# Optimization experiments

Measured on AMD Instinct MI355X. Metric: run time of the kernel, lower is better.

The kernel has to match this reference:

```python
import jax, jax.numpy as jnp
import numpy as np

NUM_CLS = 81
N_ROI = 512
N_POS = 128
OUT = 7
SAMP = 2
SCALES = (0.25, 0.125, 0.0625, 0.03125)


def _roi_align(feat, rois, out, scale, samp=SAMP):
    # feat: [C,H,W]; rois: [N,4] (x1,y1,x2,y2) in image coords. torchvision-style
    # ROIAlign, aligned=False, avg pool over samp x samp bilinear samples per bin.
    C, H, W = feat.shape
    b = rois * scale
    x1, y1, x2, y2 = b[:, 0], b[:, 1], b[:, 2], b[:, 3]
    bw = jnp.maximum(x2 - x1, 1.0) / out
    bh = jnp.maximum(y2 - y1, 1.0) / out
    N = rois.shape[0]
    # sample offsets within a roi, in bin units: [out, samp]
    grid = jnp.arange(out, dtype=feat.dtype)[:, None] + (jnp.arange(samp, dtype=feat.dtype)[None, :] + 0.5) / samp
    px = x1[:, None, None] + grid[None] * bw[:, None, None]  # [N,out,samp]
    py = y1[:, None, None] + grid[None] * bh[:, None, None]
    # full sampling grid [N, out_y, out_x, samp_y, samp_x]
    PX = jnp.broadcast_to(px[:, None, :, None, :], (N, out, out, samp, samp))
    PY = jnp.broadcast_to(py[:, :, None, :, None], (N, out, out, samp, samp))
    valid = (PX > -1.0) & (PX < W) & (PY > -1.0) & (PY < H)
    x = jnp.clip(PX, 0.0, W - 1.0)
    y = jnp.clip(PY, 0.0, H - 1.0)
    x0f = jnp.floor(x)
    y0f = jnp.floor(y)
    lx = x - x0f
    ly = y - y0f
    x0 = x0f.astype(jnp.int32)
    y0 = y0f.astype(jnp.int32)
    x1i = jnp.minimum(x0 + 1, W - 1)
    y1i = jnp.minimum(y0 + 1, H - 1)
    def g(yi, xi):
        return feat[:, yi, xi]  # [C,N,out,out,samp,samp]
    v = (g(y0, x0) * (1 - ly) * (1 - lx) + g(y0, x1i) * (1 - ly) * lx
         + g(y1i, x0) * ly * (1 - lx) + g(y1i, x1i) * ly * lx)
    v = v * valid.astype(feat.dtype)
    pooled = v.mean(axis=(-1, -2))  # [C,N,out,out]
    return pooled.transpose(1, 0, 2, 3)  # [N,C,out,out]


def setup_inputs() -> dict:
    key = jax.random.key(0)
    ks = jax.random.split(key, 16)
    H_IMG, W_IMG = 800.0, 1024.0
    P2 = jax.random.normal(ks[0], (1, 256, 200, 256), jnp.float32)
    P3 = jax.random.normal(ks[1], (1, 256, 100, 128), jnp.float32)
    P4 = jax.random.normal(ks[2], (1, 256, 50, 64), jnp.float32)
    P5 = jax.random.normal(ks[3], (1, 256, 25, 32), jnp.float32)
    x1 = jax.random.uniform(ks[4], (N_ROI,)) * (W_IMG - 64.0)
    y1 = jax.random.uniform(ks[5], (N_ROI,)) * (H_IMG - 64.0)
    w = jax.random.uniform(ks[6], (N_ROI,), minval=16.0, maxval=512.0)
    h = jax.random.uniform(ks[7], (N_ROI,), minval=16.0, maxval=512.0)
    rois = jnp.stack([x1, y1, jnp.minimum(x1 + w, W_IMG - 1.0), jnp.minimum(y1 + h, H_IMG - 1.0)], axis=-1)
    label = jax.random.randint(ks[8], (N_ROI,), 0, NUM_CLS, dtype=jnp.int32)
    loc = jax.random.normal(ks[9], (N_POS, 4), jnp.float32) * 0.1
    s = 0.02
    return {
        'P2': P2, 'P3': P3, 'P4': P4, 'P5': P5,
        'rois': rois, 'label': label, 'loc': loc,
        'W1': jax.random.normal(ks[10], (256 * OUT * OUT, 1024), jnp.float32) * s,
        'b1': jnp.zeros((1024,), jnp.float32),
        'W2': jax.random.normal(ks[11], (1024, 1024), jnp.float32) * s,
        'b2': jnp.zeros((1024,), jnp.float32),
        'Wcls': jax.random.normal(ks[12], (1024, NUM_CLS), jnp.float32) * s,
        'bcls': jnp.zeros((NUM_CLS,), jnp.float32),
        'Wloc': jax.random.normal(ks[13], (1024, NUM_CLS * 4), jnp.float32) * s,
        'bloc': jnp.zeros((NUM_CLS * 4,), jnp.float32),
    }


def reference(P2, P3, P4, P5, rois, label, loc, W1, b1, W2, b2, Wcls, bcls, Wloc, bloc):
    feats = (P2[0], P3[0], P4[0], P5[0])
    # FPN level assignment: floor(4 + log2(sqrt(area)/224)).clamp(2,5) - 2
    area = (rois[:, 2] - rois[:, 0] + 1.0) * (rois[:, 3] - rois[:, 1] + 1.0)
    lvl = jnp.floor(4.0 + jnp.log(jnp.sqrt(area) / 224.0) / np.log(2.0))
    lvl = (jnp.clip(lvl, 2.0, 5.0) - 2.0).astype(jnp.int32)  # [N] in {0,1,2,3}
    onehot = jax.nn.one_hot(lvl, 4, dtype=rois.dtype)  # [N,4]
    # pool every roi at all 4 levels, select assigned level (same values as
    # the original per-level grouping + argsort re-ordering)
    pooled = jnp.stack([_roi_align(f, rois, OUT, s) for f, s in zip(feats, SCALES)])  # [4,N,C,7,7]
    x = jnp.einsum('lnchw,nl->nchw', pooled, onehot)
    # Fast head
    x = x.reshape(x.shape[0], -1)
    h = jax.nn.relu(x @ W1 + b1)
    h = jax.nn.relu(h @ W2 + b2)
    logits = h @ Wcls + bcls                    # [N, num_cls]
    locp = (h @ Wloc + bloc).reshape(-1, NUM_CLS, 4)
    # loss assembly
    logp = jax.nn.log_softmax(logits, axis=-1)
    cls_loss = -jnp.take_along_axis(logp, label[:, None], axis=1).mean()
    loc_train = locp[jnp.arange(N_POS), label[:N_POS]]  # class-indexed gather
    t = jnp.abs(loc_train - loc)
    sl1 = jnp.where(t < 1.0, 0.5 * t * t, t - 0.5)  # SmoothL1, sigma=1
    box_loss = sl1.sum() / float(N_ROI)
    return cls_loss + box_loss
```

## Files before the change

kernel.cpp:

```cpp
#include <hip/hip_runtime.h>
#include <hip/hip_bf16.h>
#include <math.h>

#define N_ROI 512
#define N_POS 128
#define NUM_CLS 81
#define KDIM 12544
#define HID 1024

typedef __bf16 bf16x8 __attribute__((ext_vector_type(8)));
typedef __bf16 bf16x4 __attribute__((ext_vector_type(4)));
typedef float f32x4 __attribute__((ext_vector_type(4)));

__device__ inline void gload16(const void* g, void* lds) {
  __builtin_amdgcn_global_load_lds(
      (const __attribute__((address_space(1))) void*)g,
      (__attribute__((address_space(3))) void*)lds, 16, 0, 0);
}

__global__ __launch_bounds__(256) void roi_align_kernel(
    const float* __restrict__ P2, const float* __restrict__ P3,
    const float* __restrict__ P4, const float* __restrict__ P5,
    const float* __restrict__ rois, __bf16* __restrict__ xout) {
  int n = blockIdx.x;
  int ch = blockIdx.y * 4 + (threadIdx.x >> 6);
  int lane = threadIdx.x & 63;

  float rx1 = rois[n * 4 + 0], ry1 = rois[n * 4 + 1];
  float rx2 = rois[n * 4 + 2], ry2 = rois[n * 4 + 3];
  float area = (rx2 - rx1 + 1.0f) * (ry2 - ry1 + 1.0f);
  float lf = floorf(4.0f + log2f(sqrtf(area) / 224.0f));
  lf = fminf(fmaxf(lf, 2.0f), 5.0f);
  int lvl = (int)lf - 2;

  const float scales[4] = {0.25f, 0.125f, 0.0625f, 0.03125f};
  const int   Hs[4] = {200, 100, 50, 25};
  const int   Ws[4] = {256, 128, 64, 32};
  const float* feats[4] = {P2, P3, P4, P5};
  float sc = scales[lvl];
  int H = Hs[lvl], W = Ws[lvl];
  const float* feat = feats[lvl];

  float bx1 = rx1 * sc, by1 = ry1 * sc;
  float bw = fmaxf(rx2 * sc - bx1, 1.0f) * (1.0f / 7.0f);
  float bh = fmaxf(ry2 * sc - by1, 1.0f) * (1.0f / 7.0f);

  if (lane >= 49) return;
  int oh = (lane * 37) >> 8;
  int ow = lane - oh * 7;

  const float* fc = feat + (size_t)ch * H * W;
  float acc = 0.0f;
#pragma unroll
  for (int sy = 0; sy < 2; ++sy) {
    float py = by1 + ((float)oh + ((float)sy + 0.5f) * 0.5f) * bh;
    float vy = (py > -1.0f && py < (float)H) ? 1.0f : 0.0f;
    float yy = fminf(fmaxf(py, 0.0f), (float)(H - 1));
    float y0f = floorf(yy);
    int y0 = (int)y0f;
    int y1 = min(y0 + 1, H - 1);
    float ly = yy - y0f;
#pragma unroll
    for (int sx = 0; sx < 2; ++sx) {
      float px = bx1 + ((float)ow + ((float)sx + 0.5f) * 0.5f) * bw;
      float v = vy * ((px > -1.0f && px < (float)W) ? 1.0f : 0.0f);
      float xx = fminf(fmaxf(px, 0.0f), (float)(W - 1));
      float x0f = floorf(xx);
      int x0 = (int)x0f;
      int x1 = min(x0 + 1, W - 1);
      float lx = xx - x0f;
      float f00 = fc[y0 * W + x0], f01 = fc[y0 * W + x1];
      float f10 = fc[y1 * W + x0], f11 = fc[y1 * W + x1];
      float bil = f00 * (1.0f - ly) * (1.0f - lx) + f01 * (1.0f - ly) * lx +
                  f10 * ly * (1.0f - lx) + f11 * ly * lx;
      acc += bil * v;
    }
  }
  xout[(size_t)n * KDIM + (size_t)ch * 49 + lane] = (__bf16)(acc * 0.25f);
}

__global__ __launch_bounds__(256) void transpose_to_bf16_64(
    const float* __restrict__ src, __bf16* __restrict__ dst, int R, int C) {
  __shared__ float tile[64][65];
  int t = threadIdx.x;
  int bc = blockIdx.x * 64, br = blockIdx.y * 64;
  int rr = t >> 4, c4 = (t & 15) * 4;
#pragma unroll
  for (int p = 0; p < 4; ++p) {
    int r = p * 16 + rr;
    f32x4 v = *(const f32x4*)&src[(size_t)(br + r) * C + bc + c4];
    tile[r][c4] = v.x; tile[r][c4 + 1] = v.y;
    tile[r][c4 + 2] = v.z; tile[r][c4 + 3] = v.w;
  }
  __syncthreads();
#pragma unroll
  for (int p = 0; p < 4; ++p) {
    int c = p * 16 + rr;
    int r4 = c4;
    bf16x4 o = {(__bf16)tile[r4][c], (__bf16)tile[r4 + 1][c],
                (__bf16)tile[r4 + 2][c], (__bf16)tile[r4 + 3][c]};
    *(bf16x4*)&dst[(size_t)(bc + c) * R + br + r4] = o;
  }
}

__global__ __launch_bounds__(256) void transpose_pad_cls(
    const float* __restrict__ Wcls, __bf16* __restrict__ WcT) {
  __shared__ float tile[64][65];
  int t = threadIdx.x;
  int bk = blockIdx.x * 64;
  int bj = blockIdx.y * 64;
  int rr = t >> 4, c4 = (t & 15) * 4;
#pragma unroll
  for (int p = 0; p < 4; ++p) {
    int k = bk + p * 16 + rr;
#pragma unroll
    for (int i = 0; i < 4; ++i) {
      int j = bj + c4 + i;
      tile[p * 16 + rr][c4 + i] =
          (j < NUM_CLS) ? Wcls[(size_t)k * NUM_CLS + j] : 0.0f;
    }
  }
  __syncthreads();
#pragma unroll
  for (int p = 0; p < 4; ++p) {
    int c = p * 16 + rr;
    int r4 = c4;
    bf16x4 o = {(__bf16)tile[r4][c], (__bf16)tile[r4 + 1][c],
                (__bf16)tile[r4 + 2][c], (__bf16)tile[r4 + 3][c]};
    *(bf16x4*)&WcT[(size_t)(bj + c) * 1024 + bk + r4] = o;
  }
}

__global__ __launch_bounds__(256, 2) void mfma_gemm128(
    const __bf16* __restrict__ A, const __bf16* __restrict__ Bt,
    float* __restrict__ part, int M, int N, int K, int chunk) {
  __shared__ __align__(16) unsigned char smem[16384];
  unsigned char* As = smem;
  unsigned char* Bs = smem + 8192;

  int t = threadIdx.x;
  int wave = t >> 6;
  int lane = t & 63;
  int fr = lane & 15, q = lane >> 4;
  int bm = blockIdx.y * 128, bn = blockIdx.x * 128;
  int wm = (wave >> 1) * 64, wn = (wave & 1) * 64;

  int kbeg = blockIdx.z * chunk;
  int kend = min(K, kbeg + chunk);

  int qsrc = ((t & 3) - ((t >> 3) & 3)) & 3;
  const __bf16* a0 = A + (size_t)(bm + (t >> 2)) * K + kbeg + qsrc * 8;
  const __bf16* a1 = a0 + (size_t)64 * K;
  const __bf16* b0 = Bt + (size_t)(bn + (t >> 2)) * K + kbeg + qsrc * 8;
  const __bf16* b1 = b0 + (size_t)64 * K;
  unsigned char* AsW = As + wave * 1024;
  unsigned char* BsW = Bs + wave * 1024;

  int sA = ((q + (fr >> 1)) & 3) * 16;

  f32x4 acc[4][4];
#pragma unroll
  for (int i = 0; i < 4; ++i)
#pragma unroll
    for (int j = 0; j < 4; ++j) acc[i][j] = (f32x4){0.f, 0.f, 0.f, 0.f};

  for (int k0 = kbeg; k0 < kend; k0 += 32) {
    __syncthreads();
    gload16(a0, AsW);
    gload16(a1, AsW + 4096);
    gload16(b0, BsW);
    gload16(b1, BsW + 4096);
    a0 += 32; a1 += 32; b0 += 32; b1 += 32;
    __syncthreads();

    bf16x8 af[4], bfr[4];
#pragma unroll
    for (int i = 0; i < 4; ++i)
      af[i] = *(const bf16x8*)(As + (wm + 16 * i + fr) * 64 + sA);
#pragma unroll
    for (int j = 0; j < 4; ++j)
      bfr[j] = *(const bf16x8*)(Bs + (wn + 16 * j + fr) * 64 + sA);
#pragma unroll
    for (int i = 0; i < 4; ++i)
#pragma unroll
      for (int j = 0; j < 4; ++j)
        acc[i][j] = __builtin_amdgcn_mfma_f32_16x16x32_bf16(af[i], bfr[j],
                                                            acc[i][j], 0, 0, 0);
  }

  float* P = part + (size_t)blockIdx.z * M * N;
#pragma unroll
  for (int i = 0; i < 4; ++i) {
#pragma unroll
    for (int j = 0; j < 4; ++j) {
      int row0 = bm + wm + 16 * i + q * 4;
      int col = bn + wn + 16 * j + fr;
#pragma unroll
      for (int r = 0; r < 4; ++r)
        P[(size_t)(row0 + r) * N + col] = acc[i][j][r];
    }
  }
}

__global__ __launch_bounds__(256) void reduce_kernel(
    const float* __restrict__ part, int S, int MN, int Nmask,
    const float* __restrict__ bias, int bias_n, int relu,
    float* __restrict__ outf, __bf16* __restrict__ outb) {
  int i4 = (blockIdx.x * 256 + threadIdx.x) * 4;
  if (i4 >= MN) return;
  f32x4 s = {0.f, 0.f, 0.f, 0.f};
  for (int z = 0; z < S; ++z) {
    f32x4 v = *(const f32x4*)&part[(size_t)z * MN + i4];
    s.x += v.x; s.y += v.y; s.z += v.z; s.w += v.w;
  }
  int col = i4 & Nmask;
  float r[4] = {s.x, s.y, s.z, s.w};
#pragma unroll
  for (int j = 0; j < 4; ++j) {
    float b = (col + j < bias_n) ? bias[col + j] : 0.0f;
    float v = r[j] + b;
    if (relu) v = fmaxf(v, 0.0f);
    r[j] = v;
  }
  if (outf) {
    f32x4 o = {r[0], r[1], r[2], r[3]};
    *(f32x4*)&outf[i4] = o;
  }
  if (outb) {
    bf16x4 o = {(__bf16)r[0], (__bf16)r[1], (__bf16)r[2], (__bf16)r[3]};
    *(bf16x4*)&outb[i4] = o;
  }
}

__global__ __launch_bounds__(256) void loc_head_kernel(
    const float* __restrict__ h2, const float* __restrict__ Wloc,
    const float* __restrict__ bloc, const int* __restrict__ label,
    float* __restrict__ loct) {
  int n = blockIdx.x;
  int d = threadIdx.x >> 6;
  int lane = threadIdx.x & 63;
  int lab = label[n];
  const float* h = h2 + (size_t)n * HID;
  const float* w = Wloc + (size_t)lab * 4 + d;
  float s = 0.0f;
#pragma unroll
  for (int i = 0; i < 16; ++i) {
    int k = lane + i * 64;
    s += h[k] * w[(size_t)k * (NUM_CLS * 4)];
  }
#pragma unroll
  for (int off = 32; off > 0; off >>= 1) s += __shfl_down(s, off);
  if (lane == 0) loct[n * 4 + d] = s + bloc[lab * 4 + d];
}

__global__ __launch_bounds__(512) void loss_kernel(
    const float* __restrict__ logits, const int* __restrict__ label,
    const float* __restrict__ loct, const float* __restrict__ loc,
    float* __restrict__ out) {
  int t = threadIdx.x;
  const float* row = logits + (size_t)t * 128;
  float m = -1e30f;
  for (int j = 0; j < NUM_CLS; ++j) m = fmaxf(m, row[j]);
  float se = 0.0f;
  for (int j = 0; j < NUM_CLS; ++j) se += expf(row[j] - m);
  float cl = (m + logf(se)) - row[label[t]];

  float a = fabsf(loct[t] - loc[t]);
  float bl = (a < 1.0f) ? 0.5f * a * a : a - 0.5f;

  float v = cl + bl;
#pragma unroll
  for (int off = 32; off > 0; off >>= 1) v += __shfl_down(v, off);

  __shared__ float red[8];
  if ((t & 63) == 0) red[t >> 6] = v;
  __syncthreads();
  if (t == 0) {
    float tot = 0.0f;
    for (int i = 0; i < 8; ++i) tot += red[i];
    out[0] = tot * (1.0f / (float)N_ROI);
  }
}

extern "C" void kernel_launch(void* const* d_in, const int* in_sizes, int n_in,
                              void* d_out, int out_size, void* d_ws, size_t ws_size,
                              hipStream_t stream) {
  const float* P2   = (const float*)d_in[0];
  const float* P3   = (const float*)d_in[1];
  const float* P4   = (const float*)d_in[2];
  const float* P5   = (const float*)d_in[3];
  const float* rois = (const float*)d_in[4];
  const int*   label= (const int*)d_in[5];
  const float* loc  = (const float*)d_in[6];
  const float* W1   = (const float*)d_in[7];
  const float* b1   = (const float*)d_in[8];
  const float* W2   = (const float*)d_in[9];
  const float* b2   = (const float*)d_in[10];
  const float* Wcls = (const float*)d_in[11];
  const float* bcls = (const float*)d_in[12];
  const float* Wloc = (const float*)d_in[13];
  const float* bloc = (const float*)d_in[14];
  float* out = (float*)d_out;

  char* w = (char*)d_ws;
  __bf16* xb  = (__bf16*)w;  w += (size_t)N_ROI * KDIM * 2;
  __bf16* W1t = (__bf16*)w;  w += (size_t)KDIM * HID * 2;
  __bf16* W2t = (__bf16*)w;  w += (size_t)HID * HID * 2;
  __bf16* WcT = (__bf16*)w;  w += (size_t)128 * HID * 2;
  __bf16* h1b = (__bf16*)w;  w += (size_t)N_ROI * HID * 2;
  __bf16* h2b = (__bf16*)w;  w += (size_t)N_ROI * HID * 2;
  float*  h2f = (float*)w;   w += (size_t)N_ROI * HID * 4;
  float*  logits = (float*)w; w += (size_t)N_ROI * 128 * 4;
  float*  loct = (float*)w;  w += (size_t)N_ROI * 4;
  float*  part = (float*)w;

  transpose_to_bf16_64<<<dim3(HID / 64, KDIM / 64), 256, 0, stream>>>(W1, W1t,
                                                                      KDIM, HID);
  transpose_to_bf16_64<<<dim3(HID / 64, HID / 64), 256, 0, stream>>>(W2, W2t,
                                                                     HID, HID);
  transpose_pad_cls<<<dim3(16, 2), 256, 0, stream>>>(Wcls, WcT);
  roi_align_kernel<<<dim3(N_ROI, 64), 256, 0, stream>>>(P2, P3, P4, P5, rois,
                                                        xb);

  mfma_gemm128<<<dim3(HID / 128, N_ROI / 128, 16), 256, 0, stream>>>(
      xb, W1t, part, N_ROI, HID, KDIM, 800);
  reduce_kernel<<<(N_ROI * HID) / 1024, 256, 0, stream>>>(
      part, 16, N_ROI * HID, HID - 1, b1, HID, 1, nullptr, h1b);

  mfma_gemm128<<<dim3(HID / 128, N_ROI / 128, 8), 256, 0, stream>>>(
      h1b, W2t, part, N_ROI, HID, HID, 128);
  reduce_kernel<<<(N_ROI * HID) / 1024, 256, 0, stream>>>(
      part, 8, N_ROI * HID, HID - 1, b2, HID, 1, h2f, h2b);

  mfma_gemm128<<<dim3(1, N_ROI / 128, 4), 256, 0, stream>>>(
      h2b, WcT, part, N_ROI, 128, HID, 256);
  reduce_kernel<<<(N_ROI * 128) / 1024, 256, 0, stream>>>(
      part, 4, N_ROI * 128, 127, bcls, NUM_CLS, 0, logits, nullptr);

  loc_head_kernel<<<N_POS, 256, 0, stream>>>(h2f, Wloc, bloc, label, loct);
  loss_kernel<<<1, 512, 0, stream>>>(logits, label, loct, loc, out);
}
```

Before: 319.7 us.

## Precompute ROI sample coordinates in LDS and pack threads densely in roi_align

The ROI-align kernel now computes the 14 x- and 14 y-sample indices and weights once per ROI into shared memory. Threads then walk a dense flattened channel×cell index, so no lanes idle (before, 15 of 64 did), and the grid shrinks from 64 to 7 blocks per ROI with 7 outputs per thread. Bilinear math is rewritten with lerps and byte offsets. Separately, the W1/W2 transpose writes 8 bf16 values per store instead of 4, giving wider stores. The cost is an added __syncthreads and LDS reads per output.

After: 362.2 us. +13.3%, slower.

```diff
diff --git a/kernel.cpp b/kernel.cpp
--- a/kernel.cpp
+++ b/kernel.cpp
@@ -23,8 +23,13 @@
     const float* __restrict__ P4, const float* __restrict__ P5,
     const float* __restrict__ rois, __bf16* __restrict__ xout) {
   int n = blockIdx.x;
-  int ch = blockIdx.y * 4 + (threadIdx.x >> 6);
-  int lane = threadIdx.x & 63;
+  int t = threadIdx.x;
+
+  __shared__ int2   gxi[14];
+  __shared__ float2 gxf[14];
+  __shared__ int2   gyi[14];
+  __shared__ float2 gyf[14];
+  __shared__ int    s_lvl, s_HWb;
 
   float rx1 = rois[n * 4 + 0], ry1 = rois[n * 4 + 1];
   float rx2 = rois[n * 4 + 2], ry2 = rois[n * 4 + 3];
@@ -36,47 +41,86 @@
   const float scales[4] = {0.25f, 0.125f, 0.0625f, 0.03125f};
   const int   Hs[4] = {200, 100, 50, 25};
   const int   Ws[4] = {256, 128, 64, 32};
-  const float* feats[4] = {P2, P3, P4, P5};
   float sc = scales[lvl];
   int H = Hs[lvl], W = Ws[lvl];
-  const float* feat = feats[lvl];
 
   float bx1 = rx1 * sc, by1 = ry1 * sc;
   float bw = fmaxf(rx2 * sc - bx1, 1.0f) * (1.0f / 7.0f);
   float bh = fmaxf(ry2 * sc - by1, 1.0f) * (1.0f / 7.0f);
 
-  if (lane >= 49) return;
-  int oh = (lane * 37) >> 8;
-  int ow = lane - oh * 7;
-
-  const float* fc = feat + (size_t)ch * H * W;
-  float acc = 0.0f;
-#pragma unroll
-  for (int sy = 0; sy < 2; ++sy) {
-    float py = by1 + ((float)oh + ((float)sy + 0.5f) * 0.5f) * bh;
+  if (t < 14) {
+    int i = t >> 1, j = t & 1;
+    float g = (float)i + 0.25f + 0.5f * (float)j;
+    float px = bx1 + g * bw;
+    float vx = (px > -1.0f && px < (float)W) ? 1.0f : 0.0f;
+    float xx = fminf(fmaxf(px, 0.0f), (float)(W - 1));
+    float x0f = floorf(xx);
+    int x0 = (int)x0f;
+    int x1 = min(x0 + 1, W - 1);
+    gxi[t] = make_int2(x0 * 4, x1 * 4);
+    gxf[t] = make_float2(xx - x0f, vx);
+    if (t == 0) { s_lvl = lvl; s_HWb = H * W * 4; }
+  } else if (t >= 64 && t < 78) {
+    int s = t - 64;
+    int i = s >> 1, j = s & 1;
+    float g = (float)i + 0.25f + 0.5f * (float)j;
+    float py = by1 + g * bh;
     float vy = (py > -1.0f && py < (float)H) ? 1.0f : 0.0f;
     float yy = fminf(fmaxf(py, 0.0f), (float)(H - 1));
     float y0f = floorf(yy);
     int y0 = (int)y0f;
     int y1 = min(y0 + 1, H - 1);
-    float ly = yy - y0f;
-#pragma unroll
-    for (int sx = 0; sx < 2; ++sx) {
-      float px = bx1 + ((float)ow + ((float)sx + 0.5f) * 0.5f) * bw;
-      float v = vy * ((px > -1.0f && px < (float)W) ? 1.0f : 0.0f);
-      float xx = fminf(fmaxf(px, 0.0f), (float)(W - 1));
-      float x0f = floorf(xx);
-      int x0 = (int)x0f;
-      int x1 = min(x0 + 1, W - 1);
-      float lx = xx - x0f;
-      float f00 = fc[y0 * W + x0], f01 = fc[y0 * W + x1];
-      float f10 = fc[y1 * W + x0], f11 = fc[y1 * W + x1];
-      float bil = f00 * (1.0f - ly) * (1.0f - lx) + f01 * (1.0f - ly) * lx +
-                  f10 * ly * (1.0f - lx) + f11 * ly * lx;
-      acc += bil * v;
+    gyi[s] = make_int2(y0 * W * 4, y1 * W * 4);
+    gyf[s] = make_float2(yy - y0f, vy);
+  }
+  __syncthreads();
+
+  int lvl_s = __builtin_amdgcn_readfirstlane(s_lvl);
+  const char* base = (const char*)(lvl_s == 0 ? P2 : lvl_s == 1 ? P3
+                                   : lvl_s == 2 ? P4 : P5);
+  int HWb = s_HWb;
+
+  int idx0 = blockIdx.y * 1792 + t;
+  __bf16* outn = xout + (size_t)n * KDIM;
+
+#pragma unroll
+  for (int i = 0; i < 7; ++i) {
+    int idx = idx0 + i * 256;
+    int c = (idx * 42800) >> 21;
+    int cell = idx - c * 49;
+    int oh = (cell * 37) >> 8;
+    int ow = cell - oh * 7;
+
+    int4 xi = *(const int4*)&gxi[2 * ow];
+    float4 xf = *(const float4*)&gxf[2 * ow];
+    int4 yi = *(const int4*)&gyi[2 * oh];
+    float4 yf = *(const float4*)&gyf[2 * oh];
+
+    int cb = c * HWb;
+    float acc = 0.0f;
+#pragma unroll
+    for (int sy = 0; sy < 2; ++sy) {
+      int by0 = sy ? yi.z : yi.x;
+      int by1 = sy ? yi.w : yi.y;
+      float ly = sy ? yf.z : yf.x;
+      float vy = sy ? yf.w : yf.y;
+#pragma unroll
+      for (int sx = 0; sx < 2; ++sx) {
+        int bx0 = sx ? xi.z : xi.x;
+        int bx1 = sx ? xi.w : xi.y;
+        float lx = sx ? xf.z : xf.x;
+        float v = vy * (sx ? xf.w : xf.y);
+        float f00 = *(const float*)(base + (cb + by0 + bx0));
+        float f01 = *(const float*)(base + (cb + by0 + bx1));
+        float f10 = *(const float*)(base + (cb + by1 + bx0));
+        float f11 = *(const float*)(base + (cb + by1 + bx1));
+        float fx0 = f00 + lx * (f01 - f00);
+        float fx1 = f10 + lx * (f11 - f10);
+        acc += (fx0 + ly * (fx1 - fx0)) * v;
+      }
     }
-  }
-  xout[(size_t)n * KDIM + (size_t)ch * 49 + lane] = (__bf16)(acc * 0.25f);
+    outn[idx] = (__bf16)(acc * 0.25f);
+  }
 }
 
 __global__ __launch_bounds__(256) void transpose_to_bf16_64(
@@ -94,12 +138,14 @@
   }
   __syncthreads();
 #pragma unroll
-  for (int p = 0; p < 4; ++p) {
-    int c = p * 16 + rr;
-    int r4 = c4;
-    bf16x4 o = {(__bf16)tile[r4][c], (__bf16)tile[r4 + 1][c],
-                (__bf16)tile[r4 + 2][c], (__bf16)tile[r4 + 3][c]};
-    *(bf16x4*)&dst[(size_t)(bc + c) * R + br + r4] = o;
+  for (int p = 0; p < 2; ++p) {
+    int group = t + 256 * p;
+    int c = group >> 3;
+    int r0 = (group & 7) * 8;
+    bf16x8 o;
+#pragma unroll
+    for (int j = 0; j < 8; ++j) o[j] = (__bf16)tile[r0 + j][c];
+    *(bf16x8*)&dst[(size_t)(bc + c) * R + br + r0] = o;
   }
 }
 
@@ -319,8 +365,8 @@
   transpose_to_bf16_64<<<dim3(HID / 64, HID / 64), 256, 0, stream>>>(W2, W2t,
                                                                      HID, HID);
   transpose_pad_cls<<<dim3(16, 2), 256, 0, stream>>>(Wcls, WcT);
-  roi_align_kernel<<<dim3(N_ROI, 64), 256, 0, stream>>>(P2, P3, P4, P5, rois,
-                                                        xb);
+  roi_align_kernel<<<dim3(N_ROI, 7), 256, 0, stream>>>(P2, P3, P4, P5, rois,
+                                                       xb);
 
   mfma_gemm128<<<dim3(HID / 128, N_ROI / 128, 16), 256, 0, stream>>>(
       xb, W1t, part, N_ROI, HID, KDIM, 800);
```
